# Performance work log

Measured on AMD Instinct MI355X. Metric: run time of the kernel, lower is better.

The kernel has to match this reference:

```python
import jax, jax.numpy as jnp
import numpy as np

B, S, H = 1, 2048, 2048
NH, NKV, HD = 32, 8, 64
GROUPS = NH // NKV
KV_DIM = NKV * HD
COMP = int(S * 0.5)
FF = 5632  # round_up(2048*4*2/3, 256), fla GatedMLP convention
DEPTH = 2
EPS = 1e-6


def rmsnorm(x, w):
    var = jnp.mean(jnp.square(x), axis=-1, keepdims=True)
    return x * jax.lax.rsqrt(var + EPS) * w


def setup_inputs() -> dict:
    key = jax.random.key(0)
    ks = jax.random.split(key, 10)
    sc = 0.02
    return {
        "hidden_states": jax.random.normal(ks[0], (B, S, H), jnp.float32),
        "comp_w": jax.random.normal(ks[1], (COMP, S), jnp.float32) * sc,
        "comp_b": jnp.zeros((COMP,), jnp.float32),
        "q_w": jax.random.normal(ks[2], (H, H), jnp.float32) * sc,
        "k_w": jax.random.normal(ks[3], (KV_DIM, H), jnp.float32) * sc,
        "v_w": jax.random.normal(ks[4], (KV_DIM, H), jnp.float32) * sc,
        "o_w": jax.random.normal(ks[5], (H, H), jnp.float32) * sc,
        "attn_norm_w": jnp.ones((H,), jnp.float32),
        "mlp_norm_w": jnp.ones((H,), jnp.float32),
        "gate_w": jax.random.normal(ks[6], (FF, H), jnp.float32) * sc,
        "up_w": jax.random.normal(ks[7], (FF, H), jnp.float32) * sc,
        "down_w": jax.random.normal(ks[8], (H, FF), jnp.float32) * sc,
    }


def reference(hidden_states, comp_w, comp_b, q_w, k_w, v_w, o_w,
              attn_norm_w, mlp_norm_w, gate_w, up_w, down_w):
    # init_compressed_tokens: Linear over the sequence axis
    # (b,s,h) -> transpose -> (b,h,s) @ W^T -> (b,h,c) -> transpose -> (b,c,h)
    compressed = jnp.einsum('bsh,cs->bch', hidden_states, comp_w) + comp_b[None, :, None]

    for _ in range(DEPTH):
        residual = jnp.concatenate([hidden_states, compressed], axis=1)  # (b, s+c, h)
        ct = rmsnorm(compressed, attn_norm_w)
        q = (ct @ q_w.T).reshape(B, COMP, NH, HD)
        k = (residual @ k_w.T).reshape(B, S + COMP, NKV, HD)
        v = (residual @ v_w.T).reshape(B, S + COMP, NKV, HD)
        # GQA expand (repeat_interleave along head dim)
        k = jnp.repeat(k, GROUPS, axis=2)
        v = jnp.repeat(v, GROUPS, axis=2)
        scores = jnp.einsum('bsnk,btnk->bsnt', q, k) / (HD ** 0.5)
        attn = jax.nn.softmax(scores, axis=-1)
        o = jnp.einsum('bsnt,btnk->bsnk', attn, v).reshape(B, COMP, H)
        compressed = o @ o_w.T + ct
        ct2 = rmsnorm(compressed, mlp_norm_w)
        mlp_out = (jax.nn.silu(ct2 @ gate_w.T) * (ct2 @ up_w.T)) @ down_w.T
        compressed = mlp_out + ct2
    return compressed
```

## Files before the change

kernel.cpp:

```cpp
#include <hip/hip_runtime.h>
#include <math.h>

constexpr int S_   = 2048;
constexpr int H_   = 2048;
constexpr int NH_  = 32;
constexpr int NKV_ = 8;
constexpr int HD_  = 64;
constexpr int GROUPS_ = NH_ / NKV_;
constexpr int KV_  = NKV_ * HD_;
constexpr int KV2_ = 2 * KV_;
constexpr int COMP_ = 1024;
constexpr int FF_  = 5632;
constexpr int GU2_ = 2 * FF_;
constexpr int TOT_ = S_ + COMP_;
constexpr float EPS_ = 1e-6f;
constexpr int SK_ = 4;
constexpr int SP_ = 2;
constexpr float LOG2E_ = 1.44269504088896340736f;

typedef __attribute__((ext_vector_type(4))) float f32x4;
typedef __attribute__((ext_vector_type(8))) short bf16x8;
typedef __attribute__((ext_vector_type(8))) ushort u16x8;

__device__ __forceinline__ ushort f2bf(float x) {
    union { float f; unsigned u; } v; v.f = x;
    unsigned r = v.u + 0x7fffu + ((v.u >> 16) & 1u);
    return (ushort)(r >> 16);
}
__device__ __forceinline__ float bf2f(ushort x) {
    union { unsigned u; float f; } v; v.u = ((unsigned)x) << 16;
    return v.f;
}

__global__ __launch_bounds__(256) void f2b_k(
    const float* __restrict__ x, ushort* __restrict__ y, int n4)
{
    int i = blockIdx.x * 256 + threadIdx.x;
    const int stride = gridDim.x * 256;
    for (; i < n4; i += stride) {
        float4 v = ((const float4*)x)[i];
        ushort4 r = {f2bf(v.x), f2bf(v.y), f2bf(v.z), f2bf(v.w)};
        ((ushort4*)y)[i] = r;
    }
}

__global__ __launch_bounds__(256) void tpose64(
    const ushort* __restrict__ in, ushort* __restrict__ out,
    int R, int C, int ldi)
{
    __shared__ ushort T[64][72];
    const int r0 = blockIdx.x * 64, c0 = blockIdx.y * 64;
    const int row = threadIdx.x >> 2, seg = threadIdx.x & 3;

    const ushort* g = &in[(size_t)(r0 + row) * ldi + c0 + seg * 16];
    *(u16x8*)&T[row][seg * 16]     = *(const u16x8*)g;
    *(u16x8*)&T[row][seg * 16 + 8] = *(const u16x8*)(g + 8);
    __syncthreads();

    ushort tmp[16];
#pragma unroll
    for (int j = 0; j < 16; j++) tmp[j] = T[seg * 16 + j][row];
    ushort* go = &out[(size_t)(c0 + row) * R + r0 + seg * 16];
    *(u16x8*)go       = *(const u16x8*)&tmp[0];
    *(u16x8*)(go + 8) = *(const u16x8*)&tmp[8];
}

__global__ __launch_bounds__(256) void mfma_gemm(
    const ushort* __restrict__ A, const ushort* __restrict__ B,
    const float* __restrict__ addp, const float* __restrict__ bias,
    float oscale, float* __restrict__ outf, ushort* __restrict__ outb,
    int M, int N, int K)
{
    __shared__ ushort Alds[128 * 32];
    __shared__ ushort Blds[128 * 32];

    const int tid  = threadIdx.x;
    const int w    = tid >> 6;
    const int lane = tid & 63;
    const int bm = blockIdx.y, bn = blockIdx.x;
    const int wr = w >> 1, wc = w & 1;
    const int fr = lane & 15;
    const int fq = lane >> 4;
    const int srow = lane >> 2;
    const int skof = (lane & 3) * 8;

    f32x4 acc[4][4];
#pragma unroll
    for (int i = 0; i < 4; i++)
#pragma unroll
        for (int j = 0; j < 4; j++)
            acc[i][j] = (f32x4){0.f, 0.f, 0.f, 0.f};

    for (int k0 = 0; k0 < K; k0 += 32) {
        __syncthreads();
#pragma unroll
        for (int i = 0; i < 2; i++) {
            const int slot = w * 2 + i;
            const ushort* ga = &A[(size_t)(bm * 128 + slot * 16 + srow) * K + k0 + skof];
            __builtin_amdgcn_global_load_lds(
                (const __attribute__((address_space(1))) void*)ga,
                (__attribute__((address_space(3))) void*)&Alds[slot * 512], 16, 0, 0);
            const ushort* gb = &B[(size_t)(bn * 128 + slot * 16 + srow) * K + k0 + skof];
            __builtin_amdgcn_global_load_lds(
                (const __attribute__((address_space(1))) void*)gb,
                (__attribute__((address_space(3))) void*)&Blds[slot * 512], 16, 0, 0);
        }
        __syncthreads();

        bf16x8 a[4], b[4];
#pragma unroll
        for (int mt = 0; mt < 4; mt++)
            a[mt] = *(const bf16x8*)&Alds[(wr * 64 + mt * 16 + fr) * 32 + fq * 8];
#pragma unroll
        for (int nt = 0; nt < 4; nt++)
            b[nt] = *(const bf16x8*)&Blds[(wc * 64 + nt * 16 + fr) * 32 + fq * 8];

#pragma unroll
        for (int mt = 0; mt < 4; mt++)
#pragma unroll
            for (int nt = 0; nt < 4; nt++)
                acc[mt][nt] = __builtin_amdgcn_mfma_f32_16x16x32_bf16(
                    a[mt], b[nt], acc[mt][nt], 0, 0, 0);
    }

#pragma unroll
    for (int mt = 0; mt < 4; mt++) {
#pragma unroll
        for (int nt = 0; nt < 4; nt++) {
#pragma unroll
            for (int r = 0; r < 4; r++) {
                const int row = bm * 128 + wr * 64 + mt * 16 + fq * 4 + r;
                const int col = bn * 128 + wc * 64 + nt * 16 + fr;
                float v = acc[mt][nt][r] * oscale;
                if (bias) v += bias[row];
                if (addp) v += addp[(size_t)row * N + col];
                if (outf) outf[(size_t)row * N + col] = v;
                if (outb) outb[(size_t)row * N + col] = f2bf(v);
            }
        }
    }
}

__global__ __launch_bounds__(256) void mfma_gemm_sk(
    const ushort* __restrict__ A, const ushort* __restrict__ B,
    float* __restrict__ part, int M, int N, int K, int Kc)
{
    __shared__ ushort Alds[128 * 32];
    __shared__ ushort Blds[128 * 32];

    const int tid  = threadIdx.x;
    const int w    = tid >> 6;
    const int lane = tid & 63;
    const int bm = blockIdx.y, bn = blockIdx.x, z = blockIdx.z;
    const int wr = w >> 1, wc = w & 1;
    const int fr = lane & 15;
    const int fq = lane >> 4;
    const int srow = lane >> 2;
    const int skof = (lane & 3) * 8;

    f32x4 acc[4][4];
#pragma unroll
    for (int i = 0; i < 4; i++)
#pragma unroll
        for (int j = 0; j < 4; j++)
            acc[i][j] = (f32x4){0.f, 0.f, 0.f, 0.f};

    const int kbeg = z * Kc;
    for (int k0 = kbeg; k0 < kbeg + Kc; k0 += 32) {
        __syncthreads();
#pragma unroll
        for (int i = 0; i < 2; i++) {
            const int slot = w * 2 + i;
            const ushort* ga = &A[(size_t)(bm * 128 + slot * 16 + srow) * K + k0 + skof];
            __builtin_amdgcn_global_load_lds(
                (const __attribute__((address_space(1))) void*)ga,
                (__attribute__((address_space(3))) void*)&Alds[slot * 512], 16, 0, 0);
            const ushort* gb = &B[(size_t)(bn * 128 + slot * 16 + srow) * K + k0 + skof];
            __builtin_amdgcn_global_load_lds(
                (const __attribute__((address_space(1))) void*)gb,
                (__attribute__((address_space(3))) void*)&Blds[slot * 512], 16, 0, 0);
        }
        __syncthreads();

        bf16x8 a[4], b[4];
#pragma unroll
        for (int mt = 0; mt < 4; mt++)
            a[mt] = *(const bf16x8*)&Alds[(wr * 64 + mt * 16 + fr) * 32 + fq * 8];
#pragma unroll
        for (int nt = 0; nt < 4; nt++)
            b[nt] = *(const bf16x8*)&Blds[(wc * 64 + nt * 16 + fr) * 32 + fq * 8];

#pragma unroll
        for (int mt = 0; mt < 4; mt++)
#pragma unroll
            for (int nt = 0; nt < 4; nt++)
                acc[mt][nt] = __builtin_amdgcn_mfma_f32_16x16x32_bf16(
                    a[mt], b[nt], acc[mt][nt], 0, 0, 0);
    }

    float* pz = part + (size_t)z * M * N;
#pragma unroll
    for (int mt = 0; mt < 4; mt++)
#pragma unroll
        for (int nt = 0; nt < 4; nt++)
#pragma unroll
            for (int r = 0; r < 4; r++) {
                const int row = bm * 128 + wr * 64 + mt * 16 + fq * 4 + r;
                const int col = bn * 128 + wc * 64 + nt * 16 + fr;
                pz[(size_t)row * N + col] = acc[mt][nt][r];
            }
}

__global__ __launch_bounds__(256) void sk_reduce(
    const float* __restrict__ part, int mn4, int n4,
    const float* __restrict__ bias, const float* __restrict__ addp,
    float oscale, float* __restrict__ outf, ushort* __restrict__ outb)
{
    const size_t mn = (size_t)mn4 * 4;
    int i = blockIdx.x * 256 + threadIdx.x;
    const int stride = gridDim.x * 256;
    for (; i < mn4; i += stride) {
        float4 v = ((const float4*)part)[i];
#pragma unroll
        for (int z = 1; z < SK_; z++) {
            const float4 pz = ((const float4*)(part + z * mn))[i];
            v.x += pz.x; v.y += pz.y; v.z += pz.z; v.w += pz.w;
        }
        v.x *= oscale; v.y *= oscale; v.z *= oscale; v.w *= oscale;
        if (bias) {
            const float bb = bias[i / n4];
            v.x += bb; v.y += bb; v.z += bb; v.w += bb;
        }
        if (addp) {
            const float4 ad = ((const float4*)addp)[i];
            v.x += ad.x; v.y += ad.y; v.z += ad.z; v.w += ad.w;
        }
        if (outf) ((float4*)outf)[i] = v;
        if (outb) {
            ushort4 r = {f2bf(v.x), f2bf(v.y), f2bf(v.z), f2bf(v.w)};
            ((ushort4*)outb)[i] = r;
        }
    }
}

__global__ __launch_bounds__(256) void attn_mfma(
    const ushort* __restrict__ q, const ushort* __restrict__ k, int ldk,
    const ushort* __restrict__ vt, float* __restrict__ attp,
    float* __restrict__ ml)
{
    constexpr int LDT = 72;
    constexpr int KSPAN = TOT_ / SP_;
    __shared__ ushort Ks[64 * LDT];
    __shared__ ushort Vs[64 * LDT];
    __shared__ ushort Ps[64 * LDT];

    const int qt = blockIdx.x, h = blockIdx.y, z = blockIdx.z;
    const int kvh = h / GROUPS_;
    const int tid = threadIdx.x;
    const int w = tid >> 6, lane = tid & 63;
    const int fr = lane & 15, fq = lane >> 4;
    const int q0 = qt * 64;

    const ushort* qrow = &q[(size_t)(q0 + w * 16 + fr) * H_ + h * HD_];
    const bf16x8 bq0 = *(const bf16x8*)(qrow + fq * 8);
    const bf16x8 bq1 = *(const bf16x8*)(qrow + 32 + fq * 8);

    float m = -1e30f, l = 0.f;
    f32x4 acc[4];
#pragma unroll
    for (int nt = 0; nt < 4; nt++) acc[nt] = (f32x4){0.f, 0.f, 0.f, 0.f};

    const int t_beg = z * KSPAN;
    for (int t0 = t_beg; t0 < t_beg + KSPAN; t0 += 64) {
        __syncthreads();
        {
            const int row = tid >> 2, seg = tid & 3;
            const ushort* gk = &k[(size_t)(t0 + row) * ldk + kvh * HD_ + seg * 16];
            u16x8 k0v = *(const u16x8*)gk;
            u16x8 k1v = *(const u16x8*)(gk + 8);
            const ushort* gv = &vt[(size_t)(kvh * HD_ + row) * TOT_ + t0 + seg * 16];
            u16x8 v0v = *(const u16x8*)gv;
            u16x8 v1v = *(const u16x8*)(gv + 8);
            *(u16x8*)&Ks[row * LDT + seg * 16]     = k0v;
            *(u16x8*)&Ks[row * LDT + seg * 16 + 8] = k1v;
            *(u16x8*)&Vs[row * LDT + seg * 16]     = v0v;
            *(u16x8*)&Vs[row * LDT + seg * 16 + 8] = v1v;
        }
        __syncthreads();

        f32x4 st[4];
#pragma unroll
        for (int nt = 0; nt < 4; nt++) {
            bf16x8 a0 = *(const bf16x8*)&Ks[(nt * 16 + fr) * LDT + fq * 8];
            bf16x8 a1 = *(const bf16x8*)&Ks[(nt * 16 + fr) * LDT + 32 + fq * 8];
            f32x4 t = (f32x4){0.f, 0.f, 0.f, 0.f};
            t = __builtin_amdgcn_mfma_f32_16x16x32_bf16(a0, bq0, t, 0, 0, 0);
            t = __builtin_amdgcn_mfma_f32_16x16x32_bf16(a1, bq1, t, 0, 0, 0);
            st[nt] = t;
        }

        float mt = st[0][0];
#pragma unroll
        for (int nt = 0; nt < 4; nt++)
#pragma unroll
            for (int r = 0; r < 4; r++) mt = fmaxf(mt, st[nt][r]);
        mt = fmaxf(mt, __shfl_xor(mt, 16));
        mt = fmaxf(mt, __shfl_xor(mt, 32));
        const float mn = fmaxf(m, mt);
        const float alpha = exp2f(m - mn);
        m = mn;
        float ss = 0.f;
#pragma unroll
        for (int nt = 0; nt < 4; nt++)
#pragma unroll
            for (int r = 0; r < 4; r++) {
                const float pv = exp2f(st[nt][r] - mn);
                st[nt][r] = pv;
                ss += pv;
            }
        ss += __shfl_xor(ss, 16);
        ss += __shfl_xor(ss, 32);
        l = l * alpha + ss;

#pragma unroll
        for (int nt = 0; nt < 4; nt++) {
            ushort4 pk = {f2bf(st[nt][0]), f2bf(st[nt][1]),
                          f2bf(st[nt][2]), f2bf(st[nt][3])};
            *(ushort4*)&Ps[(w * 16 + fr) * LDT + nt * 16 + fq * 4] = pk;
        }

        bf16x8 ap0 = *(const bf16x8*)&Ps[(w * 16 + fr) * LDT + fq * 8];
        bf16x8 ap1 = *(const bf16x8*)&Ps[(w * 16 + fr) * LDT + 32 + fq * 8];
        float ar[4];
#pragma unroll
        for (int r = 0; r < 4; r++) ar[r] = __shfl(alpha, fq * 4 + r, 16);
#pragma unroll
        for (int nt = 0; nt < 4; nt++) {
            bf16x8 b0 = *(const bf16x8*)&Vs[(nt * 16 + fr) * LDT + fq * 8];
            bf16x8 b1 = *(const bf16x8*)&Vs[(nt * 16 + fr) * LDT + 32 + fq * 8];
            f32x4 t = acc[nt];
            t[0] *= ar[0]; t[1] *= ar[1]; t[2] *= ar[2]; t[3] *= ar[3];
            t = __builtin_amdgcn_mfma_f32_16x16x32_bf16(ap0, b0, t, 0, 0, 0);
            t = __builtin_amdgcn_mfma_f32_16x16x32_bf16(ap1, b1, t, 0, 0, 0);
            acc[nt] = t;
        }
    }

    float* pz = attp + (size_t)z * COMP_ * H_;
#pragma unroll
    for (int r = 0; r < 4; r++) {
        const int row = q0 + w * 16 + fq * 4 + r;
#pragma unroll
        for (int nt = 0; nt < 4; nt++)
            pz[(size_t)row * H_ + h * HD_ + nt * 16 + fr] = acc[nt][r];
    }
    if (lane < 16)
        ((float2*)ml)[((size_t)z * NH_ + h) * COMP_ + (q0 + w * 16 + fr)] =
            make_float2(m, l);
}

__global__ __launch_bounds__(256) void attn_merge(
    const float* __restrict__ attp, const float* __restrict__ ml,
    ushort* __restrict__ o, int n4)
{
    constexpr int H4 = H_ / 4;
    constexpr size_t PS = (size_t)COMP_ * H_;
    int i = blockIdx.x * 256 + threadIdx.x;
    const int stride = gridDim.x * 256;
    for (; i < n4; i += stride) {
        const int row = i / H4;
        const int col = (i - row * H4) * 4;
        const int h = col >> 6;
        const float2 ml0 = ((const float2*)ml)[((size_t)0 * NH_ + h) * COMP_ + row];
        const float2 ml1 = ((const float2*)ml)[((size_t)1 * NH_ + h) * COMP_ + row];
        const float M = fmaxf(ml0.x, ml1.x);
        const float a0 = exp2f(ml0.x - M), a1 = exp2f(ml1.x - M);
        const float inv = 1.0f / (a0 * ml0.y + a1 * ml1.y);
        const float4 p0 = ((const float4*)attp)[i];
        const float4 p1 = ((const float4*)(attp + PS))[i];
        ushort4 r = {f2bf((a0 * p0.x + a1 * p1.x) * inv),
                     f2bf((a0 * p0.y + a1 * p1.y) * inv),
                     f2bf((a0 * p0.z + a1 * p1.z) * inv),
                     f2bf((a0 * p0.w + a1 * p1.w) * inv)};
        ((ushort4*)o)[i] = r;
    }
}

__global__ __launch_bounds__(256) void rmsnorm_dual_k(
    const float* __restrict__ x, const float* __restrict__ w,
    float* __restrict__ y, ushort* __restrict__ yb)
{
    const int row = blockIdx.x;
    const float* xr = x + (size_t)row * H_;
    __shared__ float red[256];

    float s = 0.f;
#pragma unroll
    for (int i = 0; i < 8; i++) {
        const float v = xr[threadIdx.x + i * 256];
        s += v * v;
    }
    red[threadIdx.x] = s;
    __syncthreads();
    for (int t = 128; t > 0; t >>= 1) {
        if (threadIdx.x < t) red[threadIdx.x] += red[threadIdx.x + t];
        __syncthreads();
    }
    const float scale = rsqrtf(red[0] * (1.0f / H_) + EPS_);
#pragma unroll
    for (int i = 0; i < 8; i++) {
        const int idx = threadIdx.x + i * 256;
        const float v = xr[idx] * scale * w[idx];
        y[(size_t)row * H_ + idx] = v;
        yb[(size_t)row * H_ + idx] = f2bf(v);
    }
}

__global__ __launch_bounds__(256) void silu_mul_gu(
    const ushort* __restrict__ gu, ushort* __restrict__ g, int n4)
{
    constexpr int FF4 = FF_ / 4;
    int i = blockIdx.x * 256 + threadIdx.x;
    const int stride = gridDim.x * 256;
    for (; i < n4; i += stride) {
        const int row = i / FF4;
        const int c = (i - row * FF4) * 4;
        ushort4 gv = *(const ushort4*)&gu[(size_t)row * GU2_ + c];
        ushort4 uv = *(const ushort4*)&gu[(size_t)row * GU2_ + FF_ + c];
        float x0 = bf2f(gv.x), x1 = bf2f(gv.y), x2 = bf2f(gv.z), x3 = bf2f(gv.w);
        x0 = x0 / (1.f + __expf(-x0)) * bf2f(uv.x);
        x1 = x1 / (1.f + __expf(-x1)) * bf2f(uv.y);
        x2 = x2 / (1.f + __expf(-x2)) * bf2f(uv.z);
        x3 = x3 / (1.f + __expf(-x3)) * bf2f(uv.w);
        ushort4 r = {f2bf(x0), f2bf(x1), f2bf(x2), f2bf(x3)};
        ((ushort4*)g)[i] = r;
    }
}

extern "C" void kernel_launch(void* const* d_in, const int* in_sizes, int n_in,
                              void* d_out, int out_size, void* d_ws, size_t ws_size,
                              hipStream_t stream)
{
    (void)in_sizes; (void)n_in; (void)out_size; (void)ws_size;

    const float* hidden      = (const float*)d_in[0];
    const float* comp_w      = (const float*)d_in[1];
    const float* comp_b      = (const float*)d_in[2];
    const float* q_w         = (const float*)d_in[3];
    const float* k_w         = (const float*)d_in[4];
    const float* v_w         = (const float*)d_in[5];
    const float* o_w         = (const float*)d_in[6];
    const float* attn_norm_w = (const float*)d_in[7];
    const float* mlp_norm_w  = (const float*)d_in[8];
    const float* gate_w      = (const float*)d_in[9];
    const float* up_w        = (const float*)d_in[10];
    const float* down_w      = (const float*)d_in[11];
    float* out = (float*)d_out;

    char* p = (char*)d_ws;
    auto alloc = [&](size_t bytes) -> char* {
        char* r = p; p += (bytes + 255) & ~(size_t)255; return r;
    };
    ushort* qw_bf    = (ushort*)alloc((size_t)H_ * H_ * 2);
    ushort* kvw_bf   = (ushort*)alloc((size_t)KV2_ * H_ * 2);
    ushort* ow_bf    = (ushort*)alloc((size_t)H_ * H_ * 2);
    ushort* guw_bf   = (ushort*)alloc((size_t)GU2_ * H_ * 2);
    ushort* down_bf  = (ushort*)alloc((size_t)H_ * FF_ * 2);
    ushort* compw_bf = (ushort*)alloc((size_t)COMP_ * S_ * 2);
    ushort* hidcomp  = (ushort*)alloc((size_t)TOT_ * H_ * 2);
    ushort* hidT     = (ushort*)alloc((size_t)H_ * S_ * 2);
    ushort* ct_bf    = (ushort*)alloc((size_t)COMP_ * H_ * 2);
    ushort* ct2_bf   = (ushort*)alloc((size_t)COMP_ * H_ * 2);
    ushort* ob_bf    = (ushort*)alloc((size_t)COMP_ * H_ * 2);
    ushort* qb_bf    = (ushort*)alloc((size_t)COMP_ * H_ * 2);
    ushort* kvb_bf   = (ushort*)alloc((size_t)TOT_ * KV2_ * 2);
    ushort* vt_bf    = (ushort*)alloc((size_t)KV_ * TOT_ * 2);
    ushort* gb_bf    = (ushort*)alloc((size_t)COMP_ * FF_ * 2);
    float* comp0 = (float*)alloc((size_t)COMP_ * H_ * 4);
    float* comp1 = (float*)alloc((size_t)COMP_ * H_ * 4);
    float* ct    = (float*)alloc((size_t)COMP_ * H_ * 4);
    float* ct2   = (float*)alloc((size_t)COMP_ * H_ * 4);
    float*  skbuf = (float*)alloc((size_t)SK_ * TOT_ * KV2_ * 4);
    ushort* gub   = (ushort*)skbuf;
    float*  attp  = skbuf;
    float*  mlbuf = skbuf + (size_t)SP_ * COMP_ * H_;

    ushort* cur_bf = hidcomp + (size_t)S_ * H_;

    const dim3 blk(256);

    f2b_k<<<512, blk, 0, stream>>>(q_w,    qw_bf,            H_ * H_ / 4);
    f2b_k<<<512, blk, 0, stream>>>(k_w,    kvw_bf,           KV_ * H_ / 4);
    f2b_k<<<512, blk, 0, stream>>>(v_w,    kvw_bf + (size_t)KV_ * H_, KV_ * H_ / 4);
    f2b_k<<<512, blk, 0, stream>>>(o_w,    ow_bf,            H_ * H_ / 4);
    f2b_k<<<512, blk, 0, stream>>>(gate_w, guw_bf,           FF_ * H_ / 4);
    f2b_k<<<512, blk, 0, stream>>>(up_w,   guw_bf + (size_t)FF_ * H_, FF_ * H_ / 4);
    f2b_k<<<512, blk, 0, stream>>>(down_w, down_bf,          H_ * FF_ / 4);
    f2b_k<<<512, blk, 0, stream>>>(comp_w, compw_bf,         COMP_ * S_ / 4);
    f2b_k<<<512, blk, 0, stream>>>(hidden, hidcomp,          S_ * H_ / 4);
    tpose64<<<dim3(S_ / 64, H_ / 64), blk, 0, stream>>>(hidcomp, hidT, S_, H_, H_);

    mfma_gemm_sk<<<dim3(H_ / 128, COMP_ / 128, SK_), blk, 0, stream>>>(
        compw_bf, hidT, skbuf, COMP_, H_, S_, S_ / SK_);
    sk_reduce<<<1024, blk, 0, stream>>>(
        skbuf, COMP_ * H_ / 4, H_ / 4, comp_b, nullptr, 1.f, comp0, cur_bf);

    float* cur = comp0;
    for (int d = 0; d < 2; d++) {
        rmsnorm_dual_k<<<COMP_, blk, 0, stream>>>(cur, attn_norm_w, ct, ct_bf);

        mfma_gemm_sk<<<dim3(H_ / 128, COMP_ / 128, SK_), blk, 0, stream>>>(
            ct_bf, qw_bf, skbuf, COMP_, H_, H_, H_ / SK_);
        sk_reduce<<<1024, blk, 0, stream>>>(
            skbuf, COMP_ * H_ / 4, H_ / 4, nullptr, nullptr, 0.125f * LOG2E_,
            nullptr, qb_bf);

        mfma_gemm_sk<<<dim3(KV2_ / 128, TOT_ / 128, SK_), blk, 0, stream>>>(
            hidcomp, kvw_bf, skbuf, TOT_, KV2_, H_, H_ / SK_);
        sk_reduce<<<1024, blk, 0, stream>>>(
            skbuf, TOT_ * KV2_ / 4, KV2_ / 4, nullptr, nullptr, 1.f, nullptr, kvb_bf);

        tpose64<<<dim3(TOT_ / 64, KV_ / 64), blk, 0, stream>>>(
            kvb_bf + KV_, vt_bf, TOT_, KV_, KV2_);

        attn_mfma<<<dim3(COMP_ / 64, NH_, SP_), blk, 0, stream>>>(
            qb_bf, kvb_bf, KV2_, vt_bf, attp, mlbuf);
        attn_merge<<<512, blk, 0, stream>>>(attp, mlbuf, ob_bf, COMP_ * H_ / 4);

        mfma_gemm_sk<<<dim3(H_ / 128, COMP_ / 128, SK_), blk, 0, stream>>>(
            ob_bf, ow_bf, skbuf, COMP_, H_, H_, H_ / SK_);
        sk_reduce<<<1024, blk, 0, stream>>>(
            skbuf, COMP_ * H_ / 4, H_ / 4, nullptr, ct, 1.f, comp1, nullptr);

        rmsnorm_dual_k<<<COMP_, blk, 0, stream>>>(comp1, mlp_norm_w, ct2, ct2_bf);

        mfma_gemm<<<dim3(GU2_ / 128, COMP_ / 128), blk, 0, stream>>>(
            ct2_bf, guw_bf, nullptr, nullptr, 1.f, nullptr, gub, COMP_, GU2_, H_);

        silu_mul_gu<<<1024, blk, 0, stream>>>(gub, gb_bf, COMP_ * FF_ / 4);

        float* dst = (d == 1) ? out : comp0;
        ushort* dst_bf = (d == 1) ? nullptr : cur_bf;
        mfma_gemm_sk<<<dim3(H_ / 128, COMP_ / 128, SK_), blk, 0, stream>>>(
            gb_bf, down_bf, skbuf, COMP_, H_, FF_, FF_ / SK_);
        sk_reduce<<<1024, blk, 0, stream>>>(
            skbuf, COMP_ * H_ / 4, H_ / 4, nullptr, ct2, 1.f, dst, dst_bf);
        cur = dst;
    }
}
```

Before: 922.3 us.

## Replace gate/up GEMM with 256x256 8-wave double-buffered direct-to-LDS kernel

Adds a new GEMM kernel for the fused gate/up projection. It uses 256x256 tiles, 512 threads, and global_load_lds async copies into double-buffered, XOR-swizzled LDS. Loads are interleaved with MFMA phases and raised wave priority to hide memory latency. It also remaps block IDs to improve cache locality. In exchange it adds schedule complexity and tight barrier/vmcnt ordering that must stay correct, and it uses a large LDS footprint.

```diff
diff --git a/kernel.cpp b/kernel.cpp
--- a/kernel.cpp
+++ b/kernel.cpp
@@ -139,6 +139,163 @@
             }
         }
     }
+}
+
+#define BARS do { __builtin_amdgcn_s_barrier(); __builtin_amdgcn_sched_barrier(0); } while (0)
+#define VMW(n) asm volatile("s_waitcnt vmcnt(" #n ")" ::: "memory")
+#define STG(gp, lp) __builtin_amdgcn_global_load_lds( \
+    (const __attribute__((address_space(1))) void*)(gp), \
+    (__attribute__((address_space(3))) void*)(lp), 16, 0, 0)
+#define STA(bufA, R0, kt) STG(Ag + (size_t)(R0) * K + (kt) * 64, &(bufA)[((R0) + w * 8) * 64])
+#define STB(bufB, R0, kt) STG(Bg + (size_t)(R0) * K + (kt) * 64, &(bufB)[((R0) + w * 8) * 64])
+
+__device__ __forceinline__ void ldaq(bf16x8 (&aa)[2][2], const ushort* bufA,
+                                     int m0, int aoff, int s0, int s1)
+{
+#pragma unroll
+    for (int m = 0; m < 2; m++) {
+        aa[m][0] = *(const bf16x8*)&bufA[aoff + (m0 + m) * 1024 + s0];
+        aa[m][1] = *(const bf16x8*)&bufA[aoff + (m0 + m) * 1024 + s1];
+    }
+}
+__device__ __forceinline__ void ldbq(bf16x8 (&bb)[4][2], const ushort* bufB,
+                                     int boff, int s0, int s1)
+{
+#pragma unroll
+    for (int nt = 0; nt < 4; nt++) {
+        bb[nt][0] = *(const bf16x8*)&bufB[boff + nt * 1024 + s0];
+        bb[nt][1] = *(const bf16x8*)&bufB[boff + nt * 1024 + s1];
+    }
+}
+template <int M0>
+__device__ __forceinline__ void mfmaq(f32x4 (&acc)[8][4], bf16x8 (&aa)[2][2],
+                                      bf16x8 (&bb)[4][2])
+{
+    __builtin_amdgcn_s_setprio(1);
+#pragma unroll
+    for (int m = 0; m < 2; m++)
+#pragma unroll
+        for (int nt = 0; nt < 4; nt++) {
+            acc[M0 + m][nt] = __builtin_amdgcn_mfma_f32_16x16x32_bf16(
+                aa[m][0], bb[nt][0], acc[M0 + m][nt], 0, 0, 0);
+            acc[M0 + m][nt] = __builtin_amdgcn_mfma_f32_16x16x32_bf16(
+                aa[m][1], bb[nt][1], acc[M0 + m][nt], 0, 0, 0);
+        }
+    __builtin_amdgcn_s_setprio(0);
+}
+
+__global__ __launch_bounds__(512, 2) void gemm8ph(
+    const ushort* __restrict__ A, const ushort* __restrict__ B,
+    ushort* __restrict__ C, int N, int K)
+{
+    alignas(16) __shared__ ushort lds[4][16384];
+    ushort* const lA0 = lds[0];
+    ushort* const lB0 = lds[1];
+    ushort* const lA1 = lds[2];
+    ushort* const lB1 = lds[3];
+
+    const int tid = threadIdx.x;
+    const int w = tid >> 6, lane = tid & 63;
+    const int wr = w >> 2, wc = w & 3;
+    const int fr = lane & 15, fq = lane >> 4;
+    const int xk = fr & 7;
+
+    const int nwg = gridDim.x;
+    const int nbn = N >> 8;
+    int id = (int)blockIdx.x;
+    if (!(nwg & 7)) id = (id & 7) * (nwg >> 3) + (id >> 3);
+    const int bm = id / nbn, bn = id - bm * nbn;
+
+    const int srow = lane >> 3;
+    const int scol = ((lane & 7) ^ srow) << 3;
+    const ushort* Ag = A + (size_t)(bm * 256 + w * 8 + srow) * K + scol;
+    const ushort* Bg = B + (size_t)(bn * 256 + w * 8 + srow) * K + scol;
+
+    const int aoff = (wr * 128 + fr) * 64;
+    const int boff = (wc * 64 + fr) * 64;
+    const int s0 = ((0 + fq) ^ xk) << 3;
+    const int s1 = ((4 + fq) ^ xk) << 3;
+
+    f32x4 acc[8][4];
+#pragma unroll
+    for (int i = 0; i < 8; i++)
+#pragma unroll
+        for (int j = 0; j < 4; j++) acc[i][j] = (f32x4){0.f, 0.f, 0.f, 0.f};
+
+    bf16x8 aa[2][2], bb[4][2];
+
+    STB(lB0, 0, 0);   STB(lB0, 64, 0);
+    STA(lA0, 0, 0);   STA(lA0, 128, 0);
+    STB(lB0, 128, 0); STB(lB0, 192, 0);
+    STA(lA0, 64, 0);  STA(lA0, 192, 0);
+    STB(lB1, 0, 1);   STB(lB1, 64, 1);
+    STA(lA1, 0, 1);   STA(lA1, 128, 1);
+    STB(lB1, 128, 1); STB(lB1, 192, 1);
+    VMW(6);
+    BARS;
+
+    const int NITER = K >> 7;
+    for (int i = 0; i < NITER - 1; i++) {
+        const int t1 = 2 * i + 1, t2 = 2 * i + 2, t3 = 2 * i + 3;
+        ldbq(bb, lB0, boff, s0, s1);
+        ldaq(aa, lA0, 0, aoff, s0, s1);
+        STA(lA1, 64, t1); STA(lA1, 192, t1);
+        BARS; mfmaq<0>(acc, aa, bb); BARS;
+        ldaq(aa, lA0, 2, aoff, s0, s1);
+        STB(lB0, 0, t2); STB(lB0, 64, t2);
+        BARS; mfmaq<2>(acc, aa, bb); BARS;
+        ldaq(aa, lA0, 4, aoff, s0, s1);
+        STA(lA0, 0, t2); STA(lA0, 128, t2);
+        BARS; mfmaq<4>(acc, aa, bb); BARS;
+        ldaq(aa, lA0, 6, aoff, s0, s1);
+        STB(lB0, 128, t2); STB(lB0, 192, t2);
+        BARS; mfmaq<6>(acc, aa, bb); VMW(6); BARS;
+        ldbq(bb, lB1, boff, s0, s1);
+        ldaq(aa, lA1, 0, aoff, s0, s1);
+        STA(lA0, 64, t2); STA(lA0, 192, t2);
+        BARS; mfmaq<0>(acc, aa, bb); BARS;
+        ldaq(aa, lA1, 2, aoff, s0, s1);
+        STB(lB1, 0, t3); STB(lB1, 64, t3);
+        BARS; mfmaq<2>(acc, aa, bb); BARS;
+        ldaq(aa, lA1, 4, aoff, s0, s1);
+        STA(lA1, 0, t3); STA(lA1, 128, t3);
+        BARS; mfmaq<4>(acc, aa, bb); BARS;
+        ldaq(aa, lA1, 6, aoff, s0, s1);
+        STB(lB1, 128, t3); STB(lB1, 192, t3);
+        BARS; mfmaq<6>(acc, aa, bb); VMW(6); BARS;
+    }
+    {
+        const int t1 = 2 * NITER - 1;
+        ldbq(bb, lB0, boff, s0, s1);
+        ldaq(aa, lA0, 0, aoff, s0, s1);
+        STA(lA1, 64, t1); STA(lA1, 192, t1);
+        BARS; mfmaq<0>(acc, aa, bb); BARS;
+        ldaq(aa, lA0, 2, aoff, s0, s1);
+        BARS; mfmaq<2>(acc, aa, bb); BARS;
+        ldaq(aa, lA0, 4, aoff, s0, s1);
+        BARS; mfmaq<4>(acc, aa, bb); BARS;
+        ldaq(aa, lA0, 6, aoff, s0, s1);
+        BARS; mfmaq<6>(acc, aa, bb); VMW(0); BARS;
+        ldbq(bb, lB1, boff, s0, s1);
+        ldaq(aa, lA1, 0, aoff, s0, s1);
+        BARS; mfmaq<0>(acc, aa, bb); BARS;
+        ldaq(aa, lA1, 2, aoff, s0, s1);
+        BARS; mfmaq<2>(acc, aa, bb); BARS;
+        ldaq(aa, lA1, 4, aoff, s0, s1);
+        BARS; mfmaq<4>(acc, aa, bb); BARS;
+        ldaq(aa, lA1, 6, aoff, s0, s1);
+        mfmaq<6>(acc, aa, bb);
+    }
+
+    ushort* Cb = C + (size_t)(bm * 256 + wr * 128 + fq * 4) * N
+                   + bn * 256 + wc * 64 + fr;
+#pragma unroll
+    for (int mt = 0; mt < 8; mt++)
+#pragma unroll
+        for (int nt = 0; nt < 4; nt++)
+#pragma unroll
+            for (int r = 0; r < 4; r++)
+                Cb[(size_t)(mt * 16 + r) * N + nt * 16] = f2bf(acc[mt][nt][r]);
 }
 
 __global__ __launch_bounds__(256) void mfma_gemm_sk(
@@ -534,8 +691,8 @@
 
         rmsnorm_dual_k<<<COMP_, blk, 0, stream>>>(comp1, mlp_norm_w, ct2, ct2_bf);
 
-        mfma_gemm<<<dim3(GU2_ / 128, COMP_ / 128), blk, 0, stream>>>(
-            ct2_bf, guw_bf, nullptr, nullptr, 1.f, nullptr, gub, COMP_, GU2_, H_);
+        gemm8ph<<<dim3((GU2_ / 256) * (COMP_ / 256)), dim3(512), 0, stream>>>(
+            ct2_bf, guw_bf, gub, GU2_, H_);
 
         silu_mul_gu<<<1024, blk, 0, stream>>>(gub, gb_bf, COMP_ * FF_ / 4);
 
```

New measurement: 914.2 us. About the same (-0.9%).
